# Performance work log

Measured on AMD Instinct MI355X. Metric: run time of the kernel, lower is better.

The kernel has to match this reference:

```python
import jax, jax.numpy as jnp
import numpy as np

B, N, M, D = 256, 256, 256, 4
BIG = 1e10  # stand-in for +inf that keeps grads of unselected branches finite


def chamfer_split(target, reco, in_pid, out_pid):
    # masks of 'real' (non-zero pid) particles
    mask_x = in_pid != 0          # [B, N]
    mask_y = out_pid != 0         # [B, M]
    nx = jnp.sum(mask_x, axis=-1)  # [B] actual counts
    ny = jnp.sum(mask_y, axis=-1)
    n_in = jnp.maximum(1, nx).astype(target.dtype)   # max(1, n_in_part)
    n_out = jnp.maximum(1, ny).astype(target.dtype)  # max(1, n_out_part)

    # pairwise euclidean distances [B, N, M]
    diff = target[:, :, None, :] - reco[:, None, :, :]   # [B, N, M, D]
    dist = jnp.sqrt(jnp.sum(diff * diff, axis=-1))       # [B, N, M]

    # masked dual-axis mins (invalid entries pushed to BIG)
    min_xy = jnp.min(jnp.where(mask_y[:, None, :], dist, BIG), axis=-1)  # [B, N]
    min_yx = jnp.min(jnp.where(mask_x[:, :, None], dist, BIG), axis=-2)  # [B, M]
    sum_xy = jnp.sum(jnp.where(mask_x, min_xy, 0.0), axis=-1)  # [B]
    sum_yx = jnp.sum(jnp.where(mask_y, min_yx, 0.0), axis=-1)  # [B]

    normal = 0.5 * (sum_xy / n_out + sum_yx / n_in)  # [B]

    # edge cases: no reco non-zero particles -> sum||x_nz|| / max(1,nx);
    # no target non-zero particles -> sum over empty set = 0
    norm_x = jnp.linalg.norm(target, axis=-1)                    # [B, N]
    sum_norm_x_nz = jnp.sum(jnp.where(mask_x, norm_x, 0.0), -1)  # [B]
    eucl_non_zero = jnp.where(ny == 0, sum_norm_x_nz / n_in,
                              jnp.where(nx == 0, jnp.zeros_like(normal), normal))

    # zero-pid reco particles: mean L2 norm over zero entries
    norm_y = jnp.linalg.norm(reco, axis=-1)                          # [B, M]
    sum_norm_y_zero = jnp.sum(jnp.where(~mask_y, norm_y, 0.0), -1)   # [B]
    n_zero = jnp.maximum(1, reco.shape[1] - ny).astype(reco.dtype)
    eucl_zero = sum_norm_y_zero / n_zero

    # reduction == 'mean'
    return jnp.mean(eucl_non_zero), jnp.mean(eucl_zero)


def setup_inputs() -> dict:
    key = jax.random.key(0)
    k1, k2, k3, k4 = jax.random.split(key, 4)
    target = jax.random.normal(k1, (B, N, D), dtype=jnp.float32)
    reco = jax.random.normal(k2, (B, M, D), dtype=jnp.float32)
    in_pid = jax.random.randint(k3, (B, N), 0, 5, dtype=jnp.int32)
    out_pid = jax.random.randint(k4, (B, M), 0, 5, dtype=jnp.int32)
    return {"target": target, "reco": reco, "in_pid": in_pid, "out_pid": out_pid}


def reference(target, reco, in_pid, out_pid):
    return chamfer_split(target, reco, in_pid, out_pid)
```

## Files before the change

kernel.cpp:

```cpp
#include <hip/hip_runtime.h>
#include <math.h>

#define BB 256
#define NN 256
#define MM 256

#define POISON  1.0e18f
#define MINSENT 3.0e38f

typedef float f2 __attribute__((ext_vector_type(2)));
__device__ __forceinline__ f2 splat2(float v) { f2 r; r.x = v; r.y = v; return r; }

__global__ __launch_bounds__(1024) void chamfer_batch_kernel(
    const float* __restrict__ target,
    const float* __restrict__ reco,
    const int*   __restrict__ in_pid,
    const int*   __restrict__ out_pid,
    float2* __restrict__ ws)
{
    const int b = blockIdx.x;
    const int t = threadIdx.x;

    __shared__ __align__(16) float sTx[NN], sTy[NN], sTz[NN], sTw[NN], sTh[NN];
    __shared__ __align__(16) float sRx[MM], sRy[MM], sRz[MM], sRw[MM], sRh[MM];
    __shared__ float sRn[MM];
    __shared__ int   sMx[NN], sMy[MM];
    __shared__ float pmin1[16][NN], pmin2[16][MM];
    __shared__ int   cnt[8];
    __shared__ float wred[8][2];

    if (t < 512) {
        const bool isT = (t < 256);
        const int  i   = isT ? t : (t - 256);
        const float4* src = isT ? (const float4*)(target + (size_t)b * NN * 4)
                                : (const float4*)(reco   + (size_t)b * MM * 4);
        const int*    pid = isT ? (in_pid + b * NN) : (out_pid + b * MM);
        float4 p = src[i];
        const int m = (pid[i] != 0);
        const float rawsq = fmaf(p.x, p.x, fmaf(p.y, p.y, fmaf(p.z, p.z, p.w * p.w)));
        float4 pp = m ? p : make_float4(POISON, POISON, POISON, POISON);
        const float ppsq = m ? rawsq : (4.0f * POISON * POISON);
        if (isT) {
            sTx[i] = pp.x; sTy[i] = pp.y; sTz[i] = pp.z; sTw[i] = pp.w; sTh[i] = ppsq;
            sMx[i] = m;
        } else {
            sRx[i] = pp.x; sRy[i] = pp.y; sRz[i] = pp.z; sRw[i] = pp.w; sRh[i] = ppsq;
            sMy[i] = m;
            sRn[i] = sqrtf(rawsq);
        }
        const unsigned long long bal = __ballot(m);
        if ((t & 63) == 0) cnt[t >> 6] = (int)__popcll(bal);
    }
    __syncthreads();

    {
        const bool pass1 = (t < 512);
        const int  u = pass1 ? t : (t - 512);
        const int  c = u >> 5;
        const int  g = u & 31;
        const float* mx  = pass1 ? sTx : sRx;
        const float* my  = pass1 ? sTy : sRy;
        const float* mz  = pass1 ? sTz : sRz;
        const float* mw  = pass1 ? sTw : sRw;
        const float* ox  = pass1 ? sRx : sTx;
        const float* oy  = pass1 ? sRy : sTy;
        const float* oz  = pass1 ? sRz : sTz;
        const float* owp = pass1 ? sRw : sTw;
        float (*pout)[256] = pass1 ? pmin1 : pmin2;

        f2 n2x[8], n2y[8], n2z[8], n2w[8], mn[8];
        #pragma unroll
        for (int k = 0; k < 8; ++k) {
            const int row = g + (k << 5);
            n2x[k] = splat2(-2.f * mx[row]);
            n2y[k] = splat2(-2.f * my[row]);
            n2z[k] = splat2(-2.f * mz[row]);
            n2w[k] = splat2(-2.f * mw[row]);
            mn[k]  = splat2(MINSENT);
        }

        const int base = c << 4;
        #pragma unroll
        for (int q = 0; q < 4; ++q) {
            const int o = base + (q << 2);
            const float4 rx4 = *(const float4*)&ox[o];
            const float4 ry4 = *(const float4*)&oy[o];
            const float4 rz4 = *(const float4*)&oz[o];
            const float4 rw4 = *(const float4*)&owp[o];
            f2 rx0, rx1, ry0, ry1, rz0, rz1, rw0, rw1;
            rx0.x = rx4.x; rx0.y = rx4.y;  rx1.x = rx4.z; rx1.y = rx4.w;
            ry0.x = ry4.x; ry0.y = ry4.y;  ry1.x = ry4.z; ry1.y = ry4.w;
            rz0.x = rz4.x; rz0.y = rz4.y;  rz1.x = rz4.z; rz1.y = rz4.w;
            rw0.x = rw4.x; rw0.y = rw4.y;  rw1.x = rw4.z; rw1.y = rw4.w;
            f2 rh0 = rx0 * rx0;
            rh0 = __builtin_elementwise_fma(ry0, ry0, rh0);
            rh0 = __builtin_elementwise_fma(rz0, rz0, rh0);
            rh0 = __builtin_elementwise_fma(rw0, rw0, rh0);
            f2 rh1 = rx1 * rx1;
            rh1 = __builtin_elementwise_fma(ry1, ry1, rh1);
            rh1 = __builtin_elementwise_fma(rz1, rz1, rh1);
            rh1 = __builtin_elementwise_fma(rw1, rw1, rh1);
            #pragma unroll
            for (int k = 0; k < 8; ++k) {
                f2 a0 = __builtin_elementwise_fma(n2x[k], rx0, rh0);
                a0 = __builtin_elementwise_fma(n2y[k], ry0, a0);
                a0 = __builtin_elementwise_fma(n2z[k], rz0, a0);
                a0 = __builtin_elementwise_fma(n2w[k], rw0, a0);
                mn[k] = __builtin_elementwise_min(mn[k], a0);
                f2 a1 = __builtin_elementwise_fma(n2x[k], rx1, rh1);
                a1 = __builtin_elementwise_fma(n2y[k], ry1, a1);
                a1 = __builtin_elementwise_fma(n2z[k], rz1, a1);
                a1 = __builtin_elementwise_fma(n2w[k], rw1, a1);
                mn[k] = __builtin_elementwise_min(mn[k], a1);
            }
        }
        #pragma unroll
        for (int k = 0; k < 8; ++k)
            pout[c][g + (k << 5)] = fminf(mn[k].x, mn[k].y);
    }
    __syncthreads();

    if (t < 512) {
        const bool rows = (t < 256);
        const int  i = rows ? t : (t - 256);
        float (*pm)[256] = rows ? pmin1 : pmin2;
        float m = pm[0][i];
        #pragma unroll
        for (int c2 = 1; c2 < 16; ++c2) m = fminf(m, pm[c2][i]);
        const float hrow = rows ? sTh[i] : sRh[i];
        m = fmaxf(hrow + m, 0.0f);
        const int msk = rows ? sMx[i] : sMy[i];
        float va, vb;
        if (rows) {
            va = msk ? sqrtf(m) : 0.f;
            vb = msk ? sqrtf(sTh[i]) : 0.f;
        } else {
            va = msk ? sqrtf(m) : 0.f;
            vb = msk ? 0.f : sRn[i];
        }
        #pragma unroll
        for (int off = 32; off > 0; off >>= 1) {
            va += __shfl_down(va, off, 64);
            vb += __shfl_down(vb, off, 64);
        }
        if ((t & 63) == 0) {
            wred[t >> 6][0] = va;
            wred[t >> 6][1] = vb;
        }
    }
    __syncthreads();

    if (t == 0) {
        float s_xy = 0.f, s_nx = 0.f, s_yx = 0.f, s_ny0 = 0.f;
        int nx = 0, ny = 0;
        #pragma unroll
        for (int w = 0; w < 4; ++w) {
            s_xy  += wred[w][0];
            s_nx  += wred[w][1];
            s_yx  += wred[w + 4][0];
            s_ny0 += wred[w + 4][1];
            nx    += cnt[w];
            ny    += cnt[w + 4];
        }
        const float n_in  = (float)max(1, nx);
        const float n_out = (float)max(1, ny);
        const float normal = 0.5f * (s_xy / n_out + s_yx / n_in);
        const float eucl_nz = (ny == 0) ? (s_nx / n_in)
                                        : ((nx == 0) ? 0.0f : normal);
        const float n_zero = (float)max(1, MM - ny);
        const float eucl_z = s_ny0 / n_zero;
        ws[b] = make_float2(eucl_nz, eucl_z);
    }
}

__global__ __launch_bounds__(64) void chamfer_final_kernel(
    const float2* __restrict__ ws, float* __restrict__ out)
{
    const int t = threadIdx.x;
    float a = 0.f, z = 0.f;
    #pragma unroll
    for (int k = 0; k < 4; ++k) {
        const float2 v = ws[t + (k << 6)];
        a += v.x;
        z += v.y;
    }
    #pragma unroll
    for (int off = 32; off > 0; off >>= 1) {
        a += __shfl_down(a, off, 64);
        z += __shfl_down(z, off, 64);
    }
    if (t == 0) {
        out[0] = a * (1.0f / BB);
        out[1] = z * (1.0f / BB);
    }
}

extern "C" void kernel_launch(void* const* d_in, const int* in_sizes, int n_in,
                              void* d_out, int out_size, void* d_ws, size_t ws_size,
                              hipStream_t stream) {
    const float* target  = (const float*)d_in[0];
    const float* reco    = (const float*)d_in[1];
    const int*   in_pid  = (const int*)d_in[2];
    const int*   out_pid = (const int*)d_in[3];
    float* out = (float*)d_out;
    float2* ws = (float2*)d_ws;

    chamfer_batch_kernel<<<dim3(BB), dim3(1024), 0, stream>>>(
        target, reco, in_pid, out_pid, ws);
    chamfer_final_kernel<<<dim3(1), dim3(64), 0, stream>>>(ws, out);
}
```

Baseline: 66.45 us.

## Split each batch into two 512-thread blocks, one per min direction

Each batch is now handled by two blocks, one per reduction direction (target→reco and reco→target). Each block computes the full distance matrix but reduces along only one axis. Per-direction partial sums and counts go to a workspace, and the final kernel combines them. This doubles the block count and halves shared memory per block, which may raise occupancy across CUs, but the pairwise distances are now computed twice in total.

```diff
diff --git a/kernel.cpp b/kernel.cpp
--- a/kernel.cpp
+++ b/kernel.cpp
@@ -11,71 +11,63 @@
 typedef float f2 __attribute__((ext_vector_type(2)));
 __device__ __forceinline__ f2 splat2(float v) { f2 r; r.x = v; r.y = v; return r; }
 
-__global__ __launch_bounds__(1024) void chamfer_batch_kernel(
+__global__ __launch_bounds__(512) void chamfer_batch_kernel(
     const float* __restrict__ target,
     const float* __restrict__ reco,
     const int*   __restrict__ in_pid,
     const int*   __restrict__ out_pid,
-    float2* __restrict__ ws)
+    float4* __restrict__ ws)
 {
-    const int b = blockIdx.x;
+    const int b = blockIdx.x >> 1;
+    const int d = blockIdx.x & 1;
     const int t = threadIdx.x;
 
-    __shared__ __align__(16) float sTx[NN], sTy[NN], sTz[NN], sTw[NN], sTh[NN];
-    __shared__ __align__(16) float sRx[MM], sRy[MM], sRz[MM], sRw[MM], sRh[MM];
-    __shared__ float sRn[MM];
-    __shared__ int   sMx[NN], sMy[MM];
-    __shared__ float pmin1[16][NN], pmin2[16][MM];
-    __shared__ int   cnt[8];
-    __shared__ float wred[8][2];
+    __shared__ __align__(16) float sOx[256], sOy[256], sOz[256], sOw[256], sOh[256];
+    __shared__ __align__(16) float sSx[256], sSy[256], sSz[256], sSw[256];
+    __shared__ float sOn[256];
+    __shared__ int   sMo[256];
+    __shared__ float pmin[16][256];
+    __shared__ int   cnt[4];
+    __shared__ float wred[4][2];
 
-    if (t < 512) {
-        const bool isT = (t < 256);
-        const int  i   = isT ? t : (t - 256);
-        const float4* src = isT ? (const float4*)(target + (size_t)b * NN * 4)
-                                : (const float4*)(reco   + (size_t)b * MM * 4);
-        const int*    pid = isT ? (in_pid + b * NN) : (out_pid + b * MM);
-        float4 p = src[i];
-        const int m = (pid[i] != 0);
+    const float* ownBase  = d ? (reco   + (size_t)b * MM * 4) : (target + (size_t)b * NN * 4);
+    const float* scanBase = d ? (target + (size_t)b * NN * 4) : (reco   + (size_t)b * MM * 4);
+    const int*   ownPid   = d ? (out_pid + b * MM) : (in_pid  + b * NN);
+    const int*   scanPid  = d ? (in_pid  + b * NN) : (out_pid + b * MM);
+
+    if (t < 256) {
+        const int i = t;
+        const float4 p = ((const float4*)ownBase)[i];
+        const int m = (ownPid[i] != 0);
         const float rawsq = fmaf(p.x, p.x, fmaf(p.y, p.y, fmaf(p.z, p.z, p.w * p.w)));
-        float4 pp = m ? p : make_float4(POISON, POISON, POISON, POISON);
-        const float ppsq = m ? rawsq : (4.0f * POISON * POISON);
-        if (isT) {
-            sTx[i] = pp.x; sTy[i] = pp.y; sTz[i] = pp.z; sTw[i] = pp.w; sTh[i] = ppsq;
-            sMx[i] = m;
-        } else {
-            sRx[i] = pp.x; sRy[i] = pp.y; sRz[i] = pp.z; sRw[i] = pp.w; sRh[i] = ppsq;
-            sMy[i] = m;
-            sRn[i] = sqrtf(rawsq);
-        }
+        const float4 pp = m ? p : make_float4(POISON, POISON, POISON, POISON);
+        sOx[i] = pp.x; sOy[i] = pp.y; sOz[i] = pp.z; sOw[i] = pp.w;
+        sOh[i] = m ? rawsq : (4.0f * POISON * POISON);
+        sOn[i] = sqrtf(rawsq);
+        sMo[i] = m;
         const unsigned long long bal = __ballot(m);
         if ((t & 63) == 0) cnt[t >> 6] = (int)__popcll(bal);
+    } else {
+        const int i = t - 256;
+        const float4 p = ((const float4*)scanBase)[i];
+        const int m = (scanPid[i] != 0);
+        const float4 pp = m ? p : make_float4(POISON, POISON, POISON, POISON);
+        sSx[i] = pp.x; sSy[i] = pp.y; sSz[i] = pp.z; sSw[i] = pp.w;
     }
     __syncthreads();
 
     {
-        const bool pass1 = (t < 512);
-        const int  u = pass1 ? t : (t - 512);
-        const int  c = u >> 5;
-        const int  g = u & 31;
-        const float* mx  = pass1 ? sTx : sRx;
-        const float* my  = pass1 ? sTy : sRy;
-        const float* mz  = pass1 ? sTz : sRz;
-        const float* mw  = pass1 ? sTw : sRw;
-        const float* ox  = pass1 ? sRx : sTx;
-        const float* oy  = pass1 ? sRy : sTy;
-        const float* oz  = pass1 ? sRz : sTz;
-        const float* owp = pass1 ? sRw : sTw;
-        float (*pout)[256] = pass1 ? pmin1 : pmin2;
+        const int c = t >> 5;
+        const int g = t & 31;
 
         f2 n2x[8], n2y[8], n2z[8], n2w[8], mn[8];
         #pragma unroll
         for (int k = 0; k < 8; ++k) {
             const int row = g + (k << 5);
-            n2x[k] = splat2(-2.f * mx[row]);
-            n2y[k] = splat2(-2.f * my[row]);
-            n2z[k] = splat2(-2.f * mz[row]);
-            n2w[k] = splat2(-2.f * mw[row]);
+            n2x[k] = splat2(-2.f * sOx[row]);
+            n2y[k] = splat2(-2.f * sOy[row]);
+            n2z[k] = splat2(-2.f * sOz[row]);
+            n2w[k] = splat2(-2.f * sOw[row]);
             mn[k]  = splat2(MINSENT);
         }
 
@@ -83,10 +75,10 @@
         #pragma unroll
         for (int q = 0; q < 4; ++q) {
             const int o = base + (q << 2);
-            const float4 rx4 = *(const float4*)&ox[o];
-            const float4 ry4 = *(const float4*)&oy[o];
-            const float4 rz4 = *(const float4*)&oz[o];
-            const float4 rw4 = *(const float4*)&owp[o];
+            const float4 rx4 = *(const float4*)&sSx[o];
+            const float4 ry4 = *(const float4*)&sSy[o];
+            const float4 rz4 = *(const float4*)&sSz[o];
+            const float4 rw4 = *(const float4*)&sSw[o];
             f2 rx0, rx1, ry0, ry1, rz0, rz1, rw0, rw1;
             rx0.x = rx4.x; rx0.y = rx4.y;  rx1.x = rx4.z; rx1.y = rx4.w;
             ry0.x = ry4.x; ry0.y = ry4.y;  ry1.x = ry4.z; ry1.y = ry4.w;
@@ -116,73 +108,65 @@
         }
         #pragma unroll
         for (int k = 0; k < 8; ++k)
-            pout[c][g + (k << 5)] = fminf(mn[k].x, mn[k].y);
+            pmin[c][g + (k << 5)] = fminf(mn[k].x, mn[k].y);
     }
     __syncthreads();
 
-    if (t < 512) {
-        const bool rows = (t < 256);
-        const int  i = rows ? t : (t - 256);
-        float (*pm)[256] = rows ? pmin1 : pmin2;
-        float m = pm[0][i];
+    if (t < 256) {
+        const int i = t;
+        float m = pmin[0][i];
         #pragma unroll
-        for (int c2 = 1; c2 < 16; ++c2) m = fminf(m, pm[c2][i]);
-        const float hrow = rows ? sTh[i] : sRh[i];
-        m = fmaxf(hrow + m, 0.0f);
-        const int msk = rows ? sMx[i] : sMy[i];
-        float va, vb;
-        if (rows) {
-            va = msk ? sqrtf(m) : 0.f;
-            vb = msk ? sqrtf(sTh[i]) : 0.f;
-        } else {
-            va = msk ? sqrtf(m) : 0.f;
-            vb = msk ? 0.f : sRn[i];
-        }
+        for (int c2 = 1; c2 < 16; ++c2) m = fminf(m, pmin[c2][i]);
+        m = fmaxf(sOh[i] + m, 0.0f);
+        const int msk = sMo[i];
+        const float va = msk ? sqrtf(m) : 0.f;
+        const float vb = (d == 0) ? (msk ? sqrtf(sOh[i]) : 0.f)
+                                  : (msk ? 0.f : sOn[i]);
+        float a = va, z = vb;
         #pragma unroll
         for (int off = 32; off > 0; off >>= 1) {
-            va += __shfl_down(va, off, 64);
-            vb += __shfl_down(vb, off, 64);
+            a += __shfl_down(a, off, 64);
+            z += __shfl_down(z, off, 64);
         }
         if ((t & 63) == 0) {
-            wred[t >> 6][0] = va;
-            wred[t >> 6][1] = vb;
+            wred[t >> 6][0] = a;
+            wred[t >> 6][1] = z;
         }
     }
     __syncthreads();
 
     if (t == 0) {
-        float s_xy = 0.f, s_nx = 0.f, s_yx = 0.f, s_ny0 = 0.f;
-        int nx = 0, ny = 0;
+        float sa = 0.f, sb = 0.f;
+        int n = 0;
         #pragma unroll
         for (int w = 0; w < 4; ++w) {
-            s_xy  += wred[w][0];
-            s_nx  += wred[w][1];
-            s_yx  += wred[w + 4][0];
-            s_ny0 += wred[w + 4][1];
-            nx    += cnt[w];
-            ny    += cnt[w + 4];
+            sa += wred[w][0];
+            sb += wred[w][1];
+            n  += cnt[w];
         }
-        const float n_in  = (float)max(1, nx);
-        const float n_out = (float)max(1, ny);
-        const float normal = 0.5f * (s_xy / n_out + s_yx / n_in);
-        const float eucl_nz = (ny == 0) ? (s_nx / n_in)
-                                        : ((nx == 0) ? 0.0f : normal);
-        const float n_zero = (float)max(1, MM - ny);
-        const float eucl_z = s_ny0 / n_zero;
-        ws[b] = make_float2(eucl_nz, eucl_z);
+        ws[d * BB + b] = make_float4(sa, sb, (float)n, 0.f);
     }
 }
 
 __global__ __launch_bounds__(64) void chamfer_final_kernel(
-    const float2* __restrict__ ws, float* __restrict__ out)
+    const float4* __restrict__ ws, float* __restrict__ out)
 {
     const int t = threadIdx.x;
     float a = 0.f, z = 0.f;
     #pragma unroll
     for (int k = 0; k < 4; ++k) {
-        const float2 v = ws[t + (k << 6)];
-        a += v.x;
-        z += v.y;
+        const int bb = t + (k << 6);
+        const float4 r0 = ws[bb];
+        const float4 r1 = ws[BB + bb];
+        const int nx = (int)r0.z, ny = (int)r1.z;
+        const float n_in  = (float)max(1, nx);
+        const float n_out = (float)max(1, ny);
+        const float normal = 0.5f * (r0.x / n_out + r1.x / n_in);
+        const float eucl_nz = (ny == 0) ? (r0.y / n_in)
+                                        : ((nx == 0) ? 0.0f : normal);
+        const float n_zero = (float)max(1, MM - ny);
+        a += eucl_nz;
+        z += r1.y / n_zero;
     }
     #pragma unroll
     for (int off = 32; off > 0; off >>= 1) {
@@ -203,9 +187,9 @@
     const int*   in_pid  = (const int*)d_in[2];
     const int*   out_pid = (const int*)d_in[3];
     float* out = (float*)d_out;
-    float2* ws = (float2*)d_ws;
+    float4* ws = (float4*)d_ws;
 
-    chamfer_batch_kernel<<<dim3(BB), dim3(1024), 0, stream>>>(
+    chamfer_batch_kernel<<<dim3(2 * BB), dim3(512), 0, stream>>>(
         target, reco, in_pid, out_pid, ws);
     chamfer_final_kernel<<<dim3(1), dim3(64), 0, stream>>>(ws, out);
 }
```

Measured after the change: 67.20 us. No clear change (+1.1%).
